# Optimization experiments

Measured on AMD Instinct MI355X. Metric: run time of the kernel, lower is better.

Reference implementation:

```python
import jax, jax.numpy as jnp
import numpy as np

V, D, H, FF, L, ER_LEN = 267, 512, 8, 1024, 6, 2048
HD = D // H
NEG = -1e9


def sinusoidal_pe(S, d, dtype):
    pos = np.arange(S)[:, None].astype(np.float32)
    div = np.exp(np.arange(0, d, 2).astype(np.float32) * (-np.log(10000.0) / d))
    pe = np.zeros((S, d), dtype=np.float32)
    pe[:, 0::2] = np.sin(pos * div)
    pe[:, 1::2] = np.cos(pos * div)
    return jnp.asarray(pe, dtype=dtype)[:, None, :]  # [S,1,D]


def layernorm(x, g, b, eps=1e-5):
    mu = jnp.mean(x, -1, keepdims=True)
    var = jnp.var(x, -1, keepdims=True)
    return (x - mu) * jax.lax.rsqrt(var + eps) * g + b


def skew(qe):
    # qe: [B,H,S,S] -> Music-Transformer skew producing srel [B,H,S,S]
    S = qe.shape[-1]
    mask = jnp.flip(jnp.triu(jnp.ones((S, S), qe.dtype)), axis=0)
    qe = qe * mask
    qe = jnp.pad(qe, ((0, 0), (0, 0), (0, 0), (1, 0)))
    qe = qe.reshape(qe.shape[0], qe.shape[1], S + 1, S)
    return qe[:, :, 1:, :]


def setup_inputs() -> dict:
    key = jax.random.key(0)
    ks = jax.random.split(key, 20)
    s = 0.02
    inp = {
        'inputs_seq': jax.random.randint(ks[0], (2, 2048), 0, V),
        'emb': jax.random.normal(ks[1], (V, D)) * s,
        'in_proj_w': jax.random.normal(ks[2], (L, 3 * D, D)) * s,
        'in_proj_b': jnp.zeros((L, 3 * D)),
        'out_proj_w': jax.random.normal(ks[3], (L, D, D)) * s,
        'out_proj_b': jnp.zeros((L, D)),
        'er': jax.random.normal(ks[4], (L, ER_LEN, HD)) * s,
        'lin1_w': jax.random.normal(ks[5], (L, FF, D)) * s,
        'lin1_b': jnp.zeros((L, FF)),
        'lin2_w': jax.random.normal(ks[6], (L, D, FF)) * s,
        'lin2_b': jnp.zeros((L, D)),
        'ln1_g': jnp.ones((L, D)), 'ln1_b': jnp.zeros((L, D)),
        'ln2_g': jnp.ones((L, D)), 'ln2_b': jnp.zeros((L, D)),
        'fln_g': jnp.ones((D,)), 'fln_b': jnp.zeros((D,)),
        'wout_w': jax.random.normal(ks[7], (V, D)) * s,
        'wout_b': jnp.zeros((V,)),
    }
    return inp


def reference(inputs_seq, emb, in_proj_w, in_proj_b, out_proj_w, out_proj_b, er,
              lin1_w, lin1_b, lin2_w, lin2_b, ln1_g, ln1_b, ln2_g, ln2_b,
              fln_g, fln_b, wout_w, wout_b):
    B, S = inputs_seq.shape
    x = emb[inputs_seq]                       # [B,S,D]
    x = jnp.transpose(x, (1, 0, 2))           # [S,B,D] seq-first
    x = x + sinusoidal_pe(S, D, x.dtype)
    causal = jnp.triu(jnp.full((S, S), NEG, x.dtype), k=1)
    er_start = max(0, ER_LEN - S)
    scale = 1.0 / jnp.sqrt(jnp.asarray(HD, x.dtype))

    for i in range(L):
        qkv = jnp.einsum('sbd,ed->sbe', x, in_proj_w[i]) + in_proj_b[i]
        q, k, v = jnp.split(qkv, 3, axis=-1)
        # [S,B,D] -> [B,H,S,hd]
        def heads(t):
            return jnp.transpose(t.reshape(S, B, H, HD), (1, 2, 0, 3))
        q, k, v = heads(q) * scale, heads(k), heads(v)
        scores = jnp.einsum('bhqd,bhkd->bhqk', q, k)
        qe = jnp.einsum('bhqd,ed->bhqe', q, er[i][er_start:])
        scores = scores + skew(qe) + causal
        attn = jax.nn.softmax(scores, axis=-1)
        ctx = jnp.einsum('bhqk,bhkd->bhqd', attn, v)
        ctx = jnp.transpose(ctx, (2, 0, 1, 3)).reshape(S, B, D)
        attn_out = jnp.einsum('sbd,ed->sbe', ctx, out_proj_w[i]) + out_proj_b[i]
        x = layernorm(x + attn_out, ln1_g[i], ln1_b[i])
        h = jax.nn.relu(jnp.einsum('sbd,fd->sbf', x, lin1_w[i]) + lin1_b[i])
        ff = jnp.einsum('sbf,df->sbd', h, lin2_w[i]) + lin2_b[i]
        x = layernorm(x + ff, ln2_g[i], ln2_b[i])

    x = layernorm(x, fln_g, fln_b)
    return jnp.einsum('sbd,vd->sbv', x, wout_w) + wout_b  # [S,B,V]
```

## Files before the change

kernel.cpp:

```cpp
#include <hip/hip_runtime.h>
#include <hip/hip_bf16.h>

typedef __attribute__((ext_vector_type(4))) float f32x4;
typedef __attribute__((ext_vector_type(8))) short bf16x8;
typedef __attribute__((ext_vector_type(2))) unsigned short u16x2;
typedef __attribute__((ext_vector_type(4))) unsigned short u16x4;
typedef __attribute__((ext_vector_type(8))) unsigned short u16x8;

#define S_LEN 2048
#define BATCH 2
#define DMODEL 512
#define NHEAD 8
#define HDIM 64
#define MROWS 4096
#define LAYERS 6

#define MFMA16(a, b, c) __builtin_amdgcn_mfma_f32_16x16x32_bf16((a), (b), (c), 0, 0, 0)

__device__ __forceinline__ float bf2f(unsigned short u) {
    return __uint_as_float(((unsigned)u) << 16);
}
__device__ __forceinline__ unsigned short f2bf(float f) {
    union { float f; unsigned u; } v; v.f = f;
    unsigned r = v.u + 0x7FFF + ((v.u >> 16) & 1);
    return (unsigned short)(r >> 16);
}
__device__ __forceinline__ bf16x8 load8(const unsigned short* p) {
    return *reinterpret_cast<const bf16x8*>(p);
}

__global__ __launch_bounds__(256) void f2bf_kernel(
    const float* __restrict__ src, unsigned short* __restrict__ dst, int n8)
{
    int i = blockIdx.x * 256 + threadIdx.x;
    if (i >= n8) return;
    f32x4 a = *reinterpret_cast<const f32x4*>(src + (size_t)i * 8);
    f32x4 b = *reinterpret_cast<const f32x4*>(src + (size_t)i * 8 + 4);
    u16x8 o;
#pragma unroll
    for (int j = 0; j < 4; ++j) { o[j] = f2bf(a[j]); o[4 + j] = f2bf(b[j]); }
    *reinterpret_cast<u16x8*>(dst + (size_t)i * 8) = o;
}

__global__ __launch_bounds__(256) void embed_pe_kernel(
    const int* __restrict__ seq, const float* __restrict__ emb,
    float* __restrict__ x, unsigned short* __restrict__ x16)
{
    const int r = blockIdx.x;
    const int j = threadIdx.x;
    const int s = r >> 1, b = r & 1;
    const int tok = seq[b * S_LEN + s];
    const float e0 = emb[(size_t)tok * DMODEL + 2 * j];
    const float e1 = emb[(size_t)tok * DMODEL + 2 * j + 1];
    const double c = -9.210340371976184 / 512.0;
    double dv = exp((double)(2 * j) * c);
    double arg = (double)s * dv;
    const float v0 = e0 + (float)sin(arg);
    const float v1 = e1 + (float)cos(arg);
    x[(size_t)r * DMODEL + 2 * j]     = v0;
    x[(size_t)r * DMODEL + 2 * j + 1] = v1;
    u16x2 o; o[0] = f2bf(v0); o[1] = f2bf(v1);
    *reinterpret_cast<u16x2*>(x16 + (size_t)r * DMODEL + 2 * j) = o;
}

template<int BM>
__global__ __launch_bounds__(256) void gemm_mfma_kernel(
    const unsigned short* __restrict__ A, const unsigned short* __restrict__ W,
    const float* __restrict__ bias,
    float* __restrict__ Cf, unsigned short* __restrict__ Cb,
    unsigned short* __restrict__ vT,
    int N, int K, int relu, int qkvsplit)
{
    constexpr int MF = BM / 32;
    __shared__ __align__(16) unsigned short As[BM * 64];
    __shared__ __align__(16) unsigned short Bs[64 * 64];
    const int tid = threadIdx.x;
    const int w = tid >> 6, lane = tid & 63, l15 = lane & 15, hi = lane >> 4;
    const int wm = w >> 1, wn = w & 1;
    const int n0 = blockIdx.x * 64, m0 = blockIdx.y * BM;
    const int sr = tid >> 3;
    const int ss = tid & 7;

    bf16x8 aprf[MF], bprf[2];
    auto loadA = [&](int k0) {
#pragma unroll
        for (int i = 0; i < MF; ++i) {
            const int r = sr + 32 * i;
            aprf[i] = load8(A + (size_t)(m0 + r) * K + k0 + ((ss ^ ((r >> 1) & 7)) * 8));
        }
    };
    auto loadB = [&](int k0) {
#pragma unroll
        for (int i = 0; i < 2; ++i) {
            const int r = sr + 32 * i;
            const int nn = n0 + r;
            if (nn < N) bprf[i] = load8(W + (size_t)nn * K + k0 + ((ss ^ ((r >> 1) & 7)) * 8));
            else { u16x8 z = {0,0,0,0,0,0,0,0}; bprf[i] = *reinterpret_cast<bf16x8*>(&z); }
        }
    };

    f32x4 acc[MF][2];
#pragma unroll
    for (int mf = 0; mf < MF; ++mf)
#pragma unroll
        for (int nf = 0; nf < 2; ++nf) acc[mf][nf] = f32x4{0.f, 0.f, 0.f, 0.f};

    loadA(0); loadB(0);
    for (int k0 = 0; k0 < K; k0 += 64) {
        __syncthreads();
#pragma unroll
        for (int i = 0; i < MF; ++i)
            *reinterpret_cast<bf16x8*>(As + (sr + 32 * i) * 64 + ss * 8) = aprf[i];
#pragma unroll
        for (int i = 0; i < 2; ++i)
            *reinterpret_cast<bf16x8*>(Bs + (sr + 32 * i) * 64 + ss * 8) = bprf[i];
        if (k0 + 64 < K) { loadA(k0 + 64); loadB(k0 + 64); }
        __syncthreads();

        bf16x8 af[MF][2], bfr[2][2];
#pragma unroll
        for (int mf = 0; mf < MF; ++mf) {
            const int r = wm * (BM / 2) + mf * 16 + l15;
            const int sw = (r >> 1) & 7;
            const unsigned short* base = As + r * 64;
            af[mf][0] = *reinterpret_cast<const bf16x8*>(base + ((hi ^ sw) * 8));
            af[mf][1] = *reinterpret_cast<const bf16x8*>(base + (((hi + 4) ^ sw) * 8));
        }
#pragma unroll
        for (int nf = 0; nf < 2; ++nf) {
            const int r = wn * 32 + nf * 16 + l15;
            const int sw = (r >> 1) & 7;
            const unsigned short* base = Bs + r * 64;
            bfr[nf][0] = *reinterpret_cast<const bf16x8*>(base + ((hi ^ sw) * 8));
            bfr[nf][1] = *reinterpret_cast<const bf16x8*>(base + (((hi + 4) ^ sw) * 8));
        }
#pragma unroll
        for (int mf = 0; mf < MF; ++mf)
#pragma unroll
            for (int nf = 0; nf < 2; ++nf) {
                acc[mf][nf] = MFMA16(af[mf][0], bfr[nf][0], acc[mf][nf]);
                acc[mf][nf] = MFMA16(af[mf][1], bfr[nf][1], acc[mf][nf]);
            }
    }

#pragma unroll
    for (int nf = 0; nf < 2; ++nf) {
        const int col = n0 + wn * 32 + nf * 16 + l15;
        const bool okc = col < N;
        const float bv = okc ? bias[col] : 0.f;
#pragma unroll
        for (int mf = 0; mf < MF; ++mf) {
            const int rbase = m0 + wm * (BM / 2) + mf * 16 + hi * 4;
#pragma unroll
            for (int rg = 0; rg < 4; ++rg) {
                float v = acc[mf][nf][rg] + bv;
                if (relu) v = fmaxf(v, 0.f);
                if (okc) {
                    const int row = rbase + rg;
                    if (qkvsplit) {
                        if (col < 1024) {
                            if (col < 512) v *= 0.125f;
                            Cb[(size_t)row * 1024 + col] = f2bf(v);
                        } else {
                            const int h = (col - 1024) >> 6, d = (col - 1024) & 63;
                            const int s = row >> 1, bb = row & 1;
                            const int kt = s >> 6, kin = s & 63;
                            const int pos = (kin & 3) | (((kin >> 4) & 1) << 2)
                                          | (((kin >> 2) & 3) << 3) | (kin & 32);
                            vT[((((size_t)(bb * 8 + h) * 32 + kt) * 64 + d) << 6) + pos] = f2bf(v);
                        }
                    } else {
                        const size_t idx = (size_t)row * N + col;
                        if (Cb) Cb[idx] = f2bf(v);
                        else    Cf[idx] = v;
                    }
                }
            }
        }
    }
}

__global__ __launch_bounds__(256, 2) void attn_mfma_kernel(
    const unsigned short* __restrict__ qk16, const unsigned short* __restrict__ vT16,
    const unsigned short* __restrict__ er16,
    unsigned short* __restrict__ part16, float* __restrict__ mlbuf)
{
    __shared__ __align__(16) unsigned short K_s[64 * 64];
    __shared__ __align__(16) unsigned short V_T[64 * 64];
    __shared__ __align__(16) unsigned short Er_s[64 * 64];
    __shared__ __align__(16) unsigned short E_w[4 * 16 * 196];

    const int tid  = threadIdx.x;
    const int w    = tid >> 6;
    const int lane = tid & 63;
    const int l15  = lane & 15;
    const int hi   = lane >> 4;
    const int bx   = blockIdx.y;
    const int bh   = blockIdx.x;
    const int b    = bh >> 3, hh = bh & 7;
    const int sk   = lane;
    const int dg0  = w;
    const int dv0  = 16 * w + (lane >> 3);
    const int gv   = lane & 7;

    int qb, c;
    if (bx < 25)       { c = 0; qb = 31 - bx; }
    else if (bx < 42)  { c = 1; qb = 31 - (bx - 25); }
    else if (bx < 51)  { c = 2; qb = 31 - (bx - 42); }
    else if (bx == 51) { c = 3; qb = 31; }
    else { const int lev = (bx - 52) >> 2; c = (bx - 52) & 3; qb = 8 * c + 6 - lev; }
    const int pidx = bh * 80 + bx;
    const int q0   = qb * 64;
    const int k0s  = c * 512;
    const int ntl  = min(qb + 1 - c * 8, 8);
    const int qg   = q0 + 16 * w + l15;

    const unsigned short* qptr = qk16 + ((size_t)qg * BATCH + b) * 1024 + hh * HDIM;
    bf16x8 qf0 = load8(qptr + hi * 8);
    bf16x8 qf1 = load8(qptr + 32 + hi * 8);

    unsigned short* ewp = E_w + (w * 16 + l15) * 196;
    const int E0  = 1984 - q0 + k0s;
    const int E0m = E0 % 192;

#pragma unroll 2
    for (int mf = 0; mf < 8; ++mf) {
        int e = E0 + mf * 16 + l15;
        int ec = e > 2047 ? 2047 : e;
        bf16x8 a0 = load8(er16 + (size_t)ec * 64 + hi * 8);
        bf16x8 a1 = load8(er16 + (size_t)ec * 64 + 32 + hi * 8);
        f32x4 acc = {0.f, 0.f, 0.f, 0.f};
        acc = MFMA16(a0, qf0, acc);
        acc = MFMA16(a1, qf1, acc);
        int col = E0m + mf * 16 + 4 * hi;
        if (col >= 192) col -= 192;
        u16x4 ew;
#pragma unroll
        for (int r = 0; r < 4; ++r) ew[r] = f2bf(acc[r]);
        *reinterpret_cast<u16x4*>(ewp + col) = ew;
    }

    float m = -INFINITY, lsum = 0.f;
    f32x4 acc_o[4];
#pragma unroll
    for (int mf = 0; mf < 4; ++mf) acc_o[mf] = f32x4{0.f, 0.f, 0.f, 0.f};

    int col0t = (2047 - qg + k0s) % 192;

    bf16x8 kpr0, kpr1, vpr0, vpr1, epr0, epr1;
    {
        const unsigned short* krow = qk16 + ((size_t)(k0s + sk) * BATCH + b) * 1024 + 512 + hh * HDIM;
        kpr0 = load8(krow + dg0 * 8);       kpr1 = load8(krow + (dg0 + 4) * 8);
        const unsigned short* vbase = vT16 + (((size_t)bh * 32 + (k0s >> 6)) * 64) * 64;
        vpr0 = load8(vbase + dv0 * 64 + gv * 8);
        vpr1 = load8(vbase + (dv0 + 8) * 64 + gv * 8);
    }
    if (ntl > 1) {
        int e = E0 + 128 + sk;
        int ec = e > 2047 ? 2047 : e;
        epr0 = load8(er16 + (size_t)ec * 64 + dg0 * 8);
        epr1 = load8(er16 + (size_t)ec * 64 + (dg0 + 4) * 8);
    }

    for (int t = 0; t < ntl; ++t) {
        const int k0 = k0s + t * 64;
        const bool doE = (t + 1 < ntl);
        __syncthreads();
        *reinterpret_cast<bf16x8*>(K_s + sk * 64 + ((dg0 ^ (sk & 7)) * 8)) = kpr0;
        *reinterpret_cast<bf16x8*>(K_s + sk * 64 + (((dg0 + 4) ^ (sk & 7)) * 8)) = kpr1;
        *reinterpret_cast<bf16x8*>(V_T + dv0 * 64 + ((gv ^ (dv0 & 7)) * 8)) = vpr0;
        *reinterpret_cast<bf16x8*>(V_T + (dv0 + 8) * 64 + ((gv ^ (dv0 & 7)) * 8)) = vpr1;
        if (doE) {
            *reinterpret_cast<bf16x8*>(Er_s + sk * 64 + ((dg0 ^ (sk & 7)) * 8)) = epr0;
            *reinterpret_cast<bf16x8*>(Er_s + sk * 64 + (((dg0 + 4) ^ (sk & 7)) * 8)) = epr1;
        }
        if (t + 1 < ntl) {
            const unsigned short* krow = qk16 + ((size_t)(k0 + 64 + sk) * BATCH + b) * 1024 + 512 + hh * HDIM;
            kpr0 = load8(krow + dg0 * 8);       kpr1 = load8(krow + (dg0 + 4) * 8);
            const unsigned short* vbase = vT16 + (((size_t)bh * 32 + ((k0 + 64) >> 6)) * 64) * 64;
            vpr0 = load8(vbase + dv0 * 64 + gv * 8);
            vpr1 = load8(vbase + (dv0 + 8) * 64 + gv * 8);
            if (t + 2 < ntl) {
                int e = E0 + 128 + 64 * (t + 1) + sk;
                int ec = e > 2047 ? 2047 : e;
                epr0 = load8(er16 + (size_t)ec * 64 + dg0 * 8);
                epr1 = load8(er16 + (size_t)ec * 64 + (dg0 + 4) * 8);
            }
        }
        __syncthreads();

        f32x4 sacc[4];
#pragma unroll
        for (int f = 0; f < 4; ++f) {
            const int row = l15 + 16 * f;
            bf16x8 ka0 = *reinterpret_cast<const bf16x8*>(K_s + row * 64 + (((0 + hi) ^ (l15 & 7)) * 8));
            bf16x8 ka1 = *reinterpret_cast<const bf16x8*>(K_s + row * 64 + (((4 + hi) ^ (l15 & 7)) * 8));
            f32x4 z = {0.f, 0.f, 0.f, 0.f};
            z = MFMA16(ka0, qf0, z);
            sacc[f] = MFMA16(ka1, qf1, z);
        }

        if (doE) {
            const int fbm = (E0 + 128 + 64 * t) % 192;
#pragma unroll
            for (int mf = 0; mf < 4; ++mf) {
                const int rr = l15 + 16 * mf;
                bf16x8 a0 = *reinterpret_cast<const bf16x8*>(Er_s + rr * 64 + ((hi ^ (l15 & 7)) * 8));
                bf16x8 a1 = *reinterpret_cast<const bf16x8*>(Er_s + rr * 64 + (((hi + 4) ^ (l15 & 7)) * 8));
                f32x4 acc = {0.f, 0.f, 0.f, 0.f};
                acc = MFMA16(a0, qf0, acc);
                acc = MFMA16(a1, qf1, acc);
                int col = fbm + mf * 16 + 4 * hi;
                u16x4 ew;
#pragma unroll
                for (int r = 0; r < 4; ++r) ew[r] = f2bf(acc[r]);
                *reinterpret_cast<u16x4*>(ewp + col) = ew;
            }
        }

        float mt = -INFINITY;
#pragma unroll
        for (int f = 0; f < 4; ++f) {
#pragma unroll
            for (int r = 0; r < 4; ++r) {
                const int kk = 16 * f + 4 * hi + r;
                int col = col0t + kk;
                if (col >= 192) col -= 192;
                float sv = sacc[f][r] + bf2f(ewp[col]);
                if (k0 + kk > qg) sv = -1e9f;
                sacc[f][r] = sv;
                mt = fmaxf(mt, sv);
            }
        }
        mt = fmaxf(mt, __shfl_xor(mt, 16));
        mt = fmaxf(mt, __shfl_xor(mt, 32));
        const float mn = fmaxf(m, mt);
        const float corr = __expf(m - mn);
        float ps = 0.f;
#pragma unroll
        for (int f = 0; f < 4; ++f)
#pragma unroll
            for (int r = 0; r < 4; ++r) {
                const float e = __expf(sacc[f][r] - mn);
                sacc[f][r] = e; ps += e;
            }
        ps += __shfl_xor(ps, 16);
        ps += __shfl_xor(ps, 32);
        lsum = lsum * corr + ps;
        m = mn;

        bf16x8 pf0, pf1;
#pragma unroll
        for (int j = 0; j < 8; ++j) {
            pf0[j] = (short)f2bf(sacc[j >> 2][j & 3]);
            pf1[j] = (short)f2bf(sacc[(j >> 2) + 2][j & 3]);
        }

#pragma unroll
        for (int mf = 0; mf < 4; ++mf) {
            f32x4 a = acc_o[mf];
            a[0] *= corr; a[1] *= corr; a[2] *= corr; a[3] *= corr;
            const unsigned short* vrow = V_T + (l15 + 16 * mf) * 64;
            const int sw = l15 & 7;
            bf16x8 vf0 = *reinterpret_cast<const bf16x8*>(vrow + ((hi ^ sw) * 8));
            bf16x8 vf1 = *reinterpret_cast<const bf16x8*>(vrow + (((4 + hi) ^ sw) * 8));
            a = MFMA16(vf0, pf0, a);
            a = MFMA16(vf1, pf1, a);
            acc_o[mf] = a;
        }

        col0t += 64;
        if (col0t >= 192) col0t -= 192;
    }

    unsigned short* pa = part16 + ((size_t)pidx * 64 + 16 * w + l15) * 64;
#pragma unroll
    for (int mf = 0; mf < 4; ++mf) {
        u16x4 o;
#pragma unroll
        for (int r = 0; r < 4; ++r) o[r] = f2bf(acc_o[mf][r]);
        *reinterpret_cast<u16x4*>(pa + 16 * mf + 4 * hi) = o;
    }
    if (hi == 0) {
        float* ml = mlbuf + ((size_t)pidx * 64 + 16 * w + l15) * 2;
        ml[0] = m; ml[1] = lsum;
    }
}

__global__ __launch_bounds__(256) void attn_combine_kernel(
    const unsigned short* __restrict__ part16, const float* __restrict__ mlbuf,
    unsigned short* __restrict__ ctx16)
{
    const int flat = blockIdx.x * 256 + threadIdx.x;
    const int qi = flat >> 3, dg = flat & 7;
    const int bh = qi >> 11, ql = qi & 2047;
    const int b = bh >> 3, hh = bh & 7;
    const int qb = ql >> 6, rl = ql & 63;

    const int nch = (qb >> 3) + 1;
    float mr = -1e30f, lr = 0.f;
    float o[8];
#pragma unroll
    for (int j = 0; j < 8; ++j) o[j] = 0.f;

    for (int cc = 0; cc < nch; ++cc) {
        int idx;
        if (qb - 8 * cc >= 7) {
            const int base = (cc == 0) ? 0 : (cc == 1) ? 25 : (cc == 2) ? 42 : 51;
            idx = bh * 80 + base + (31 - qb);
        } else {
            idx = bh * 80 + 52 + 4 * (6 - (qb - 8 * cc)) + cc;
        }
        const float* ml = mlbuf + ((size_t)idx * 64 + rl) * 2;
        const float mc = ml[0], lc = ml[1];
        u16x8 a = *reinterpret_cast<const u16x8*>(part16 + ((size_t)idx * 64 + rl) * 64 + dg * 8);
        const float mn = fmaxf(mr, mc);
        const float w0 = __expf(mr - mn), w1 = __expf(mc - mn);
#pragma unroll
        for (int j = 0; j < 8; ++j) o[j] = o[j] * w0 + bf2f(a[j]) * w1;
        lr = lr * w0 + lc * w1;
        mr = mn;
    }
    const float inv = 1.f / lr;
    u16x8 res;
#pragma unroll
    for (int j = 0; j < 8; ++j) res[j] = f2bf(o[j] * inv);
    *reinterpret_cast<u16x8*>(ctx16 + ((size_t)ql * BATCH + b) * DMODEL + hh * HDIM + dg * 8) = res;
}

__global__ __launch_bounds__(256) void ln_kernel(
    const float* __restrict__ xin, const float* __restrict__ res,
    const float* __restrict__ gg, const float* __restrict__ bb,
    float* __restrict__ xout, unsigned short* __restrict__ x16out, int has_res)
{
    const int w = threadIdx.x >> 6, lane = threadIdx.x & 63;
    const int row = blockIdx.x * 4 + w;
    const float* xp = xin + (size_t)row * DMODEL + lane * 8;
    f32x4 v0 = *reinterpret_cast<const f32x4*>(xp);
    f32x4 v1 = *reinterpret_cast<const f32x4*>(xp + 4);
    if (has_res) {
        const float* rp = res + (size_t)row * DMODEL + lane * 8;
        v0 += *reinterpret_cast<const f32x4*>(rp);
        v1 += *reinterpret_cast<const f32x4*>(rp + 4);
    }
    float sum = 0.f, ssq = 0.f;
#pragma unroll
    for (int c2 = 0; c2 < 4; ++c2) {
        sum += v0[c2] + v1[c2];
        ssq += v0[c2] * v0[c2] + v1[c2] * v1[c2];
    }
#pragma unroll
    for (int off = 32; off > 0; off >>= 1) {
        sum += __shfl_xor(sum, off);
        ssq += __shfl_xor(ssq, off);
    }
    const float mu = sum * (1.f / 512.f);
    const float var = ssq * (1.f / 512.f) - mu * mu;
    const float rstd = rsqrtf(var + 1e-5f);
    f32x4 g0 = *reinterpret_cast<const f32x4*>(gg + lane * 8);
    f32x4 g1 = *reinterpret_cast<const f32x4*>(gg + lane * 8 + 4);
    f32x4 b0 = *reinterpret_cast<const f32x4*>(bb + lane * 8);
    f32x4 b1 = *reinterpret_cast<const f32x4*>(bb + lane * 8 + 4);
    f32x4 o0, o1;
    u16x8 h;
#pragma unroll
    for (int c2 = 0; c2 < 4; ++c2) {
        o0[c2] = (v0[c2] - mu) * rstd * g0[c2] + b0[c2];
        o1[c2] = (v1[c2] - mu) * rstd * g1[c2] + b1[c2];
        h[c2] = f2bf(o0[c2]); h[4 + c2] = f2bf(o1[c2]);
    }
    float* op = xout + (size_t)row * DMODEL + lane * 8;
    *reinterpret_cast<f32x4*>(op)     = o0;
    *reinterpret_cast<f32x4*>(op + 4) = o1;
    *reinterpret_cast<u16x8*>(x16out + (size_t)row * DMODEL + lane * 8) = h;
}

extern "C" void kernel_launch(void* const* d_in, const int* in_sizes, int n_in,
                              void* d_out, int out_size, void* d_ws, size_t ws_size,
                              hipStream_t stream)
{
    const int*   seq  = (const int*)d_in[0];
    const float* emb  = (const float*)d_in[1];
    const float* ipw  = (const float*)d_in[2];
    const float* ipb  = (const float*)d_in[3];
    const float* opw  = (const float*)d_in[4];
    const float* opb  = (const float*)d_in[5];
    const float* er   = (const float*)d_in[6];
    const float* l1w  = (const float*)d_in[7];
    const float* l1b  = (const float*)d_in[8];
    const float* l2w  = (const float*)d_in[9];
    const float* l2b  = (const float*)d_in[10];
    const float* ln1g = (const float*)d_in[11];
    const float* ln1b = (const float*)d_in[12];
    const float* ln2g = (const float*)d_in[13];
    const float* ln2b = (const float*)d_in[14];
    const float* flng = (const float*)d_in[15];
    const float* flnb = (const float*)d_in[16];
    const float* ww   = (const float*)d_in[17];
    const float* wb   = (const float*)d_in[18];
    float* out = (float*)d_out;

    float* xf  = (float*)d_ws;
    float* tmp = xf + (size_t)MROWS * DMODEL;
    unsigned short* x16   = (unsigned short*)(tmp + (size_t)MROWS * DMODEL);
    unsigned short* qk16  = x16  + (size_t)MROWS * DMODEL;
    unsigned short* ctx16 = qk16 + (size_t)MROWS * 1024;
    unsigned short* er16  = ctx16 + (size_t)MROWS * DMODEL;
    unsigned short* vT16  = er16 + (size_t)LAYERS * S_LEN * HDIM;
    unsigned short* w16   = vT16 + (size_t)16 * 32 * 64 * 64;
    unsigned short* h16   = qk16;
    unsigned short* part16 = (unsigned short*)tmp;
    float* mlbuf = (float*)(part16 + (size_t)1280 * 64 * 64);

    unsigned short* ipw16 = w16;
    unsigned short* opw16 = ipw16 + (size_t)LAYERS * 1536 * DMODEL;
    unsigned short* l1w16 = opw16 + (size_t)LAYERS * DMODEL * DMODEL;
    unsigned short* l2w16 = l1w16 + (size_t)LAYERS * 1024 * DMODEL;
    unsigned short* ww16  = l2w16 + (size_t)LAYERS * DMODEL * 1024;

    {
        int n8;
        n8 = LAYERS * 1536 * DMODEL / 8; f2bf_kernel<<<(n8 + 255) / 256, 256, 0, stream>>>(ipw, ipw16, n8);
        n8 = LAYERS * DMODEL * DMODEL / 8; f2bf_kernel<<<(n8 + 255) / 256, 256, 0, stream>>>(opw, opw16, n8);
        n8 = LAYERS * 1024 * DMODEL / 8; f2bf_kernel<<<(n8 + 255) / 256, 256, 0, stream>>>(l1w, l1w16, n8);
        n8 = LAYERS * DMODEL * 1024 / 8; f2bf_kernel<<<(n8 + 255) / 256, 256, 0, stream>>>(l2w, l2w16, n8);
        n8 = 267 * DMODEL / 8;           f2bf_kernel<<<(n8 + 255) / 256, 256, 0, stream>>>(ww, ww16, n8);
        n8 = LAYERS * S_LEN * HDIM / 8;  f2bf_kernel<<<(n8 + 255) / 256, 256, 0, stream>>>(er, er16, n8);
    }

    embed_pe_kernel<<<MROWS, 256, 0, stream>>>(seq, emb, xf, x16);

    for (int i = 0; i < LAYERS; ++i) {
        gemm_mfma_kernel<128><<<dim3(24, 32), 256, 0, stream>>>(
            x16, ipw16 + (size_t)i * 1536 * DMODEL, ipb + (size_t)i * 1536,
            nullptr, qk16, vT16, 1536, DMODEL, 0, 1);
        attn_mfma_kernel<<<dim3(BATCH * NHEAD, 80), 256, 0, stream>>>(
            qk16, vT16, er16 + (size_t)i * S_LEN * HDIM, part16, mlbuf);
        attn_combine_kernel<<<1024, 256, 0, stream>>>(part16, mlbuf, ctx16);
        gemm_mfma_kernel<64><<<dim3(8, 64), 256, 0, stream>>>(
            ctx16, opw16 + (size_t)i * DMODEL * DMODEL, opb + (size_t)i * DMODEL,
            tmp, nullptr, nullptr, DMODEL, DMODEL, 0, 0);
        ln_kernel<<<MROWS / 4, 256, 0, stream>>>(
            xf, tmp, ln1g + (size_t)i * DMODEL, ln1b + (size_t)i * DMODEL, xf, x16, 1);
        gemm_mfma_kernel<128><<<dim3(16, 32), 256, 0, stream>>>(
            x16, l1w16 + (size_t)i * 1024 * DMODEL, l1b + (size_t)i * 1024,
            nullptr, h16, nullptr, 1024, DMODEL, 1, 0);
        gemm_mfma_kernel<64><<<dim3(8, 64), 256, 0, stream>>>(
            h16, l2w16 + (size_t)i * DMODEL * 1024, l2b + (size_t)i * DMODEL,
            tmp, nullptr, nullptr, DMODEL, 1024, 0, 0);
        ln_kernel<<<MROWS / 4, 256, 0, stream>>>(
            xf, tmp, ln2g + (size_t)i * DMODEL, ln2b + (size_t)i * DMODEL, xf, x16, 1);
    }

    ln_kernel<<<MROWS / 4, 256, 0, stream>>>(xf, nullptr, flng, flnb, xf, x16, 0);
    gemm_mfma_kernel<64><<<dim3(5, 64), 256, 0, stream>>>(
        x16, ww16, wb, out, nullptr, nullptr, 267, DMODEL, 0, 0);
}
```

Measured before the change: 715.4 us.

## Compute per-warp relative-position band each tile from a 128-row Er ring buffer

The attention kernel drops the 192-entry circular skew buffer of bf16 q·Er products. Each warp now recomputes, per K tile, only the 80-column band of relative-position logits it needs, reading Er from a 128-row shared-memory ring that is staged up front and prefetched. The causal mask check is skipped for tiles entirely below the diagonal, and f2bf now uses the HIP intrinsic conversion. The aim is to simplify indexing and cut modulo arithmetic and E_w traffic, at the cost of recomputing five MFMA pairs per warp per tile instead of four per block-tile.

```diff
diff --git a/kernel.cpp b/kernel.cpp
--- a/kernel.cpp
+++ b/kernel.cpp
@@ -21,9 +21,8 @@
     return __uint_as_float(((unsigned)u) << 16);
 }
 __device__ __forceinline__ unsigned short f2bf(float f) {
-    union { float f; unsigned u; } v; v.f = f;
-    unsigned r = v.u + 0x7FFF + ((v.u >> 16) & 1);
-    return (unsigned short)(r >> 16);
+    __hip_bfloat16 h = __float2bfloat16(f);
+    return *reinterpret_cast<unsigned short*>(&h);
 }
 __device__ __forceinline__ bf16x8 load8(const unsigned short* p) {
     return *reinterpret_cast<const bf16x8*>(p);
@@ -187,8 +186,8 @@
 {
     __shared__ __align__(16) unsigned short K_s[64 * 64];
     __shared__ __align__(16) unsigned short V_T[64 * 64];
-    __shared__ __align__(16) unsigned short Er_s[64 * 64];
-    __shared__ __align__(16) unsigned short E_w[4 * 16 * 196];
+    __shared__ __align__(16) unsigned short Er_s[128 * 64];
+    __shared__ __align__(16) unsigned short E_w[4 * 16 * 84];
 
     const int tid  = threadIdx.x;
     const int w    = tid >> 6;
@@ -219,33 +218,25 @@
     bf16x8 qf0 = load8(qptr + hi * 8);
     bf16x8 qf1 = load8(qptr + 32 + hi * 8);
 
-    unsigned short* ewp = E_w + (w * 16 + l15) * 196;
-    const int E0  = 1984 - q0 + k0s;
-    const int E0m = E0 % 192;
-
-#pragma unroll 2
-    for (int mf = 0; mf < 8; ++mf) {
-        int e = E0 + mf * 16 + l15;
-        int ec = e > 2047 ? 2047 : e;
-        bf16x8 a0 = load8(er16 + (size_t)ec * 64 + hi * 8);
-        bf16x8 a1 = load8(er16 + (size_t)ec * 64 + 32 + hi * 8);
-        f32x4 acc = {0.f, 0.f, 0.f, 0.f};
-        acc = MFMA16(a0, qf0, acc);
-        acc = MFMA16(a1, qf1, acc);
-        int col = E0m + mf * 16 + 4 * hi;
-        if (col >= 192) col -= 192;
-        u16x4 ew;
-#pragma unroll
-        for (int r = 0; r < 4; ++r) ew[r] = f2bf(acc[r]);
-        *reinterpret_cast<u16x4*>(ewp + col) = ew;
+    unsigned short* ewp = E_w + (w * 16 + l15) * 84;
+    const int E0 = 1984 - q0 + k0s;
+
+    {
+        const int row = tid >> 1;
+        const int g4 = (tid & 1) * 4;
+        const int e = min(E0 + row, 2047);
+        const unsigned short* ep = er16 + (size_t)e * 64;
+#pragma unroll
+        for (int j = 0; j < 4; ++j) {
+            bf16x8 v = load8(ep + (g4 + j) * 8);
+            *reinterpret_cast<bf16x8*>(Er_s + row * 64 + (((g4 + j) ^ (row & 7)) * 8)) = v;
+        }
     }
 
     float m = -INFINITY, lsum = 0.f;
     f32x4 acc_o[4];
 #pragma unroll
     for (int mf = 0; mf < 4; ++mf) acc_o[mf] = f32x4{0.f, 0.f, 0.f, 0.f};
-
-    int col0t = (2047 - qg + k0s) % 192;
 
     bf16x8 kpr0, kpr1, vpr0, vpr1, epr0, epr1;
     {
@@ -255,24 +246,18 @@
         vpr0 = load8(vbase + dv0 * 64 + gv * 8);
         vpr1 = load8(vbase + (dv0 + 8) * 64 + gv * 8);
     }
-    if (ntl > 1) {
-        int e = E0 + 128 + sk;
-        int ec = e > 2047 ? 2047 : e;
-        epr0 = load8(er16 + (size_t)ec * 64 + dg0 * 8);
-        epr1 = load8(er16 + (size_t)ec * 64 + (dg0 + 4) * 8);
-    }
 
     for (int t = 0; t < ntl; ++t) {
         const int k0 = k0s + t * 64;
-        const bool doE = (t + 1 < ntl);
         __syncthreads();
         *reinterpret_cast<bf16x8*>(K_s + sk * 64 + ((dg0 ^ (sk & 7)) * 8)) = kpr0;
         *reinterpret_cast<bf16x8*>(K_s + sk * 64 + (((dg0 + 4) ^ (sk & 7)) * 8)) = kpr1;
         *reinterpret_cast<bf16x8*>(V_T + dv0 * 64 + ((gv ^ (dv0 & 7)) * 8)) = vpr0;
         *reinterpret_cast<bf16x8*>(V_T + (dv0 + 8) * 64 + ((gv ^ (dv0 & 7)) * 8)) = vpr1;
-        if (doE) {
-            *reinterpret_cast<bf16x8*>(Er_s + sk * 64 + ((dg0 ^ (sk & 7)) * 8)) = epr0;
-            *reinterpret_cast<bf16x8*>(Er_s + sk * 64 + (((dg0 + 4) ^ (sk & 7)) * 8)) = epr1;
+        if (t >= 1) {
+            const int rb = ((64 * t + 64) & 127) + sk;
+            *reinterpret_cast<bf16x8*>(Er_s + rb * 64 + ((dg0 ^ (sk & 7)) * 8)) = epr0;
+            *reinterpret_cast<bf16x8*>(Er_s + rb * 64 + (((dg0 + 4) ^ (sk & 7)) * 8)) = epr1;
         }
         if (t + 1 < ntl) {
             const unsigned short* krow = qk16 + ((size_t)(k0 + 64 + sk) * BATCH + b) * 1024 + 512 + hh * HDIM;
@@ -280,12 +265,9 @@
             const unsigned short* vbase = vT16 + (((size_t)bh * 32 + ((k0 + 64) >> 6)) * 64) * 64;
             vpr0 = load8(vbase + dv0 * 64 + gv * 8);
             vpr1 = load8(vbase + (dv0 + 8) * 64 + gv * 8);
-            if (t + 2 < ntl) {
-                int e = E0 + 128 + 64 * (t + 1) + sk;
-                int ec = e > 2047 ? 2047 : e;
-                epr0 = load8(er16 + (size_t)ec * 64 + dg0 * 8);
-                epr1 = load8(er16 + (size_t)ec * 64 + (dg0 + 4) * 8);
-            }
+            const int e = min(E0 + 64 * t + 128 + sk, 2047);
+            epr0 = load8(er16 + (size_t)e * 64 + dg0 * 8);
+            epr1 = load8(er16 + (size_t)e * 64 + (dg0 + 4) * 8);
         }
         __syncthreads();
 
@@ -300,34 +282,33 @@
             sacc[f] = MFMA16(ka1, qf1, z);
         }
 
-        if (doE) {
-            const int fbm = (E0 + 128 + 64 * t) % 192;
-#pragma unroll
-            for (int mf = 0; mf < 4; ++mf) {
-                const int rr = l15 + 16 * mf;
-                bf16x8 a0 = *reinterpret_cast<const bf16x8*>(Er_s + rr * 64 + ((hi ^ (l15 & 7)) * 8));
-                bf16x8 a1 = *reinterpret_cast<const bf16x8*>(Er_s + rr * 64 + (((hi + 4) ^ (l15 & 7)) * 8));
-                f32x4 acc = {0.f, 0.f, 0.f, 0.f};
-                acc = MFMA16(a0, qf0, acc);
-                acc = MFMA16(a1, qf1, acc);
-                int col = fbm + mf * 16 + 4 * hi;
-                u16x4 ew;
-#pragma unroll
-                for (int r = 0; r < 4; ++r) ew[r] = f2bf(acc[r]);
-                *reinterpret_cast<u16x4*>(ewp + col) = ew;
-            }
-        }
-
+#pragma unroll
+        for (int g = 0; g < 5; ++g) {
+            const int rg = (48 - 16 * w + 16 * g + 64 * t) & 127;
+            const int row = (rg + l15) & 127;
+            const unsigned short* eb = Er_s + row * 64;
+            bf16x8 a0 = *reinterpret_cast<const bf16x8*>(eb + ((hi ^ (l15 & 7)) * 8));
+            bf16x8 a1 = *reinterpret_cast<const bf16x8*>(eb + (((hi + 4) ^ (l15 & 7)) * 8));
+            f32x4 qe = {0.f, 0.f, 0.f, 0.f};
+            qe = MFMA16(a0, qf0, qe);
+            qe = MFMA16(a1, qf1, qe);
+            u16x4 ew;
+#pragma unroll
+            for (int r = 0; r < 4; ++r) ew[r] = f2bf(qe[r]);
+            *reinterpret_cast<u16x4*>(ewp + 16 * g + 4 * hi) = ew;
+        }
+        __builtin_amdgcn_sched_barrier(0);
+
+        const unsigned short* gwp = ewp + (15 - l15);
+        const bool needmask = (k0 + 63 > q0 + 16 * w);
         float mt = -INFINITY;
 #pragma unroll
         for (int f = 0; f < 4; ++f) {
 #pragma unroll
             for (int r = 0; r < 4; ++r) {
                 const int kk = 16 * f + 4 * hi + r;
-                int col = col0t + kk;
-                if (col >= 192) col -= 192;
-                float sv = sacc[f][r] + bf2f(ewp[col]);
-                if (k0 + kk > qg) sv = -1e9f;
+                float sv = sacc[f][r] + bf2f(gwp[kk]);
+                if (needmask && (k0 + kk > qg)) sv = -1e9f;
                 sacc[f][r] = sv;
                 mt = fmaxf(mt, sv);
             }
@@ -368,9 +349,6 @@
             a = MFMA16(vf1, pf1, a);
             acc_o[mf] = a;
         }
-
-        col0t += 64;
-        if (col0t >= 192) col0t -= 192;
     }
 
     unsigned short* pa = part16 + ((size_t)pidx * 64 + 16 * w + l15) * 64;
```

Result: no change. 712.6 us (-0.4%).
